# Kernel tuning notes

Measured on AMD Instinct MI355X. Metric: run time of the kernel, lower is better.

The kernel has to match this reference:

```python
import jax, jax.numpy as jnp
import numpy as np

N_NODE, N_REL = 200000, 64
DIM, N_FACTOR, N_LAYER, K, B = 64, 4, 2, 32, 1024


def setup_inputs() -> dict:
    key = jax.random.key(0)
    ks = jax.random.split(key, 12)
    node_emb = jax.random.normal(ks[0], (N_NODE, N_FACTOR, DIM), jnp.float32) * 0.05
    relation_emb = jax.random.normal(ks[1], (N_REL, N_FACTOR, DIM), jnp.float32) * 0.05
    # attention MLP: Linear(2d -> d), ReLU, Linear(d -> 1); stored as [in, out]
    W1 = jax.random.normal(ks[2], (2 * DIM, DIM), jnp.float32) * (1.0 / np.sqrt(2 * DIM))
    b1 = jnp.zeros((DIM,), jnp.float32)
    W2 = jax.random.normal(ks[3], (DIM, 1), jnp.float32) * (1.0 / np.sqrt(DIM))
    b2 = jnp.zeros((1,), jnp.float32)
    users = jax.random.randint(ks[4], (B,), 0, N_NODE)
    items = jax.random.randint(ks[5], (B,), 0, N_NODE)

    def make_triple(kh, kr, kt):
        h = jax.random.randint(kh, (B, 1, N_LAYER, K), 0, N_NODE)
        r = jax.random.randint(kr, (B, 1, N_LAYER, K), 0, N_REL)
        t = jax.random.randint(kt, (B, 1, N_LAYER, K), 0, N_NODE)
        return jnp.concatenate([h, r, t], axis=1)  # [B, 3, L, K]

    users_triple = make_triple(ks[6], ks[7], ks[8])
    items_triple = make_triple(ks[9], ks[10], ks[11])
    return {
        "node_emb": node_emb, "relation_emb": relation_emb,
        "W1": W1, "b1": b1, "W2": W2, "b2": b2,
        "users": users, "items": items,
        "users_triple": users_triple, "items_triple": items_triple,
    }


def _knowledge_attention(h_emb, t_emb, W1, b1, W2, b2):
    # h_emb, t_emb: [B, L, K, F, d]
    x = jnp.concatenate([h_emb, t_emb], axis=-1)          # [B,L,K,F,2d]
    hid = jax.nn.relu(x @ W1 + b1)                        # [B,L,K,F,d]
    logits = jnp.squeeze(hid @ W2 + b2, axis=-1)          # [B,L,K,F]
    w = jax.nn.softmax(logits, axis=2)                    # softmax over neighbors K
    return jnp.sum(w[..., None] * t_emb, axis=2)          # [B,L,F,d]


def _tower(node_emb, idx, triple, W1, b1, W2, b2):
    origin = node_emb[idx]                                # [B,F,d]
    h = node_emb[triple[:, 0]]                            # [B,L,K,F,d]
    t = node_emb[triple[:, 2]]                            # [B,L,K,F,d]
    layers = _knowledge_attention(h, t, W1, b1, W2, b2)   # [B,L,F,d]
    emb = jnp.concatenate([origin[:, None], layers], axis=1)  # [B,L+1,F,d]
    return jnp.transpose(emb, (1, 0, 2, 3))               # [L+1,B,F,d]


def reference(node_emb, relation_emb, W1, b1, W2, b2, users, items, users_triple, items_triple):
    # relation_emb is gathered in the original but never used by the attention math.
    u = _tower(node_emb, users, users_triple, W1, b1, W2, b2)
    v = _tower(node_emb, items, items_triple, W1, b1, W2, b2)
    return jnp.stack([u, v])  # [2, L+1, B, F, d]
```

## Files before the change

### kernel.cpp

```cpp
#include <hip/hip_runtime.h>
#include <math.h>

#define NNODE  200000
#define DIM    64
#define NF     4
#define NLAYER 2
#define KK     32
#define BB     1024

typedef __bf16 bf16x8 __attribute__((ext_vector_type(8)));
typedef float  f32x4  __attribute__((ext_vector_type(4)));

__global__ void prep_w1t(const float* __restrict__ W1, __bf16* __restrict__ w1t) {
    int j = blockIdx.x * 256 + threadIdx.x;
    int d = j >> 7, i = j & 127;
    w1t[j] = (__bf16)W1[i * 64 + d];
}

__global__ __launch_bounds__(256, 4) void kgat_direct(
    const float* __restrict__ node_emb,
    const __bf16* __restrict__ w1t,
    const float* __restrict__ b1,
    const float* __restrict__ W2,
    const int*   __restrict__ users,
    const int*   __restrict__ items,
    const int*   __restrict__ users_triple,
    const int*   __restrict__ items_triple,
    float*       __restrict__ out)
{
    __shared__ float logitS[128];
    __shared__ float outS[256];

    const int bid   = blockIdx.x;
    const int tower = bid >> 11;
    const int b     = (bid >> 1) & 1023;
    const int layer = bid & 1;
    const int tid   = threadIdx.x;
    const int w     = tid >> 6;
    const int lane  = tid & 63;
    const int m16   = lane & 15;
    const int quad  = lane >> 4;

    const int* __restrict__ triple = tower ? items_triple : users_triple;
    const int* __restrict__ idxarr = tower ? items : users;

    const int hbase = ((b * 3 + 0) * NLAYER + layer) * KK;
    const int tbase = ((b * 3 + 2) * NLAYER + layer) * KK;

    int hi[2], ti[2];
    hi[0] = triple[hbase + m16];
    hi[1] = triple[hbase + 16 + m16];
    ti[0] = triple[tbase + m16];
    ti[1] = triple[tbase + 16 + m16];

    bf16x8 Af[2][4];
#pragma unroll
    for (int mt = 0; mt < 2; ++mt) {
        const float* __restrict__ rh = node_emb + ((size_t)hi[mt] * NF + w) * DIM;
        const float* __restrict__ rt = node_emb + ((size_t)ti[mt] * NF + w) * DIM;
#pragma unroll
        for (int kt = 0; kt < 4; ++kt) {
            const float* __restrict__ src = (kt < 2 ? rh : rt) + (kt & 1) * 32 + quad * 8;
            f32x4 v0 = *(const f32x4*)src;
            f32x4 v1 = *(const f32x4*)(src + 4);
            bf16x8 a;
#pragma unroll
            for (int u = 0; u < 4; ++u) { a[u] = (__bf16)v0[u]; a[4 + u] = (__bf16)v1[u]; }
            Af[mt][kt] = a;
        }
    }

    f32x4 C[2][4];
#pragma unroll
    for (int mt = 0; mt < 2; ++mt)
#pragma unroll
        for (int nt = 0; nt < 4; ++nt) C[mt][nt] = (f32x4)(0.f);

#pragma unroll
    for (int kt = 0; kt < 4; ++kt) {
        bf16x8 Bn[4];
#pragma unroll
        for (int nt = 0; nt < 4; ++nt)
            Bn[nt] = *(const bf16x8*)(w1t + (nt * 16 + m16) * 128 + kt * 32 + quad * 8);
#pragma unroll
        for (int nt = 0; nt < 4; ++nt) {
            C[0][nt] = __builtin_amdgcn_mfma_f32_16x16x32_bf16(Af[0][kt], Bn[nt], C[0][nt], 0, 0, 0);
            C[1][nt] = __builtin_amdgcn_mfma_f32_16x16x32_bf16(Af[1][kt], Bn[nt], C[1][nt], 0, 0, 0);
        }
    }

    float b1v[4], w2v[4];
#pragma unroll
    for (int nt = 0; nt < 4; ++nt) {
        b1v[nt] = b1[nt * 16 + m16];
        w2v[nt] = W2[nt * 16 + m16];
    }
    float lsum[2][4];
#pragma unroll
    for (int mt = 0; mt < 2; ++mt)
#pragma unroll
        for (int r = 0; r < 4; ++r) {
            float s = 0.f;
#pragma unroll
            for (int nt = 0; nt < 4; ++nt)
                s += fmaxf(C[mt][nt][r] + b1v[nt], 0.f) * w2v[nt];
            lsum[mt][r] = s;
        }
#pragma unroll
    for (int off = 1; off < 16; off <<= 1)
#pragma unroll
        for (int mt = 0; mt < 2; ++mt)
#pragma unroll
            for (int r = 0; r < 4; ++r)
                lsum[mt][r] += __shfl_xor(lsum[mt][r], off, 64);

    if (m16 == 0) {
#pragma unroll
        for (int mt = 0; mt < 2; ++mt) {
            f32x4 v;
#pragma unroll
            for (int r = 0; r < 4; ++r) v[r] = lsum[mt][r];
            *(f32x4*)&logitS[w * 32 + mt * 16 + quad * 4] = v;
        }
    }
    const float lg = logitS[w * 32 + (lane & 31)];

    float mx = lg;
#pragma unroll
    for (int off = 16; off; off >>= 1) mx = fmaxf(mx, __shfl_xor(mx, off, 64));
    const float e = __expf(lg - mx);
    float s = e;
#pragma unroll
    for (int off = 16; off; off >>= 1) s += __shfl_xor(s, off, 64);
    const float wgt = e / s;

    float o0[8], o1[8];
#pragma unroll
    for (int j = 0; j < 8; ++j) { o0[j] = 0.f; o1[j] = 0.f; }
#pragma unroll
    for (int mt = 0; mt < 2; ++mt) {
        const float wv = __shfl(wgt, mt * 16 + m16, 64);
#pragma unroll
        for (int j = 0; j < 8; ++j) {
            o0[j] += wv * (float)Af[mt][2][j];
            o1[j] += wv * (float)Af[mt][3][j];
        }
    }
#pragma unroll
    for (int off = 1; off < 16; off <<= 1)
#pragma unroll
        for (int j = 0; j < 8; ++j) {
            o0[j] += __shfl_xor(o0[j], off, 64);
            o1[j] += __shfl_xor(o1[j], off, 64);
        }
    if (m16 == 0) {
        f32x4 v;
#pragma unroll
        for (int j = 0; j < 4; ++j) v[j] = o0[j];
        *(f32x4*)&outS[w * 64 + quad * 8] = v;
#pragma unroll
        for (int j = 0; j < 4; ++j) v[j] = o0[4 + j];
        *(f32x4*)&outS[w * 64 + quad * 8 + 4] = v;
#pragma unroll
        for (int j = 0; j < 4; ++j) v[j] = o1[j];
        *(f32x4*)&outS[w * 64 + 32 + quad * 8] = v;
#pragma unroll
        for (int j = 0; j < 4; ++j) v[j] = o1[4 + j];
        *(f32x4*)&outS[w * 64 + 32 + quad * 8 + 4] = v;
    }
    out[(((size_t)(tower * 3 + 1 + layer) * BB + b) * NF + w) * DIM + lane] =
        outS[w * 64 + lane];

    if (layer == 0) {
        const int oid = idxarr[b];
        out[(((size_t)(tower * 3 + 0) * BB + b) * NF + w) * DIM + lane] =
            node_emb[((size_t)oid * NF + w) * DIM + lane];
    }
}

extern "C" void kernel_launch(void* const* d_in, const int* in_sizes, int n_in,
                              void* d_out, int out_size, void* d_ws, size_t ws_size,
                              hipStream_t stream) {
    const float* node_emb     = (const float*)d_in[0];
    const float* W1           = (const float*)d_in[2];
    const float* b1           = (const float*)d_in[3];
    const float* W2           = (const float*)d_in[4];
    const float* b2           = (const float*)d_in[5]; (void)b2;
    const int*   users        = (const int*)d_in[6];
    const int*   items        = (const int*)d_in[7];
    const int*   users_triple = (const int*)d_in[8];
    const int*   items_triple = (const int*)d_in[9];
    float* out = (float*)d_out;

    __bf16* w1t = (__bf16*)d_ws;

    hipLaunchKernelGGL(prep_w1t, dim3(32), dim3(256), 0, stream, W1, w1t);
    hipLaunchKernelGGL(kgat_direct, dim3(2 * BB * NLAYER), dim3(256), 0, stream,
                       node_emb, w1t, b1, W2,
                       users, items, users_triple, items_triple, out);
}
```

Baseline: 304.0 us.

## Process both layers per block with prefetch of next layer's gathers

Each block now handles both layers for one (tower, batch) pair instead of one layer. The gather of layer 1's head and tail rows is issued before layer 0's compute, so memory latency overlaps with the MFMA and softmax work. W1 fragments are loaded once into registers and reused across both layers, and the LDS staging of outputs is replaced by direct vector stores from lane 0 of each 16-lane group. In exchange the grid is halved, register pressure rises (launch bounds drop from 4 to 3 blocks per CU), and a dead Bn load is left in.

```diff
diff --git a/kernel.cpp b/kernel.cpp
--- a/kernel.cpp
+++ b/kernel.cpp
@@ -17,7 +17,7 @@
     w1t[j] = (__bf16)W1[i * 64 + d];
 }
 
-__global__ __launch_bounds__(256, 4) void kgat_direct(
+__global__ __launch_bounds__(256, 3) void kgat_pipe(
     const float* __restrict__ node_emb,
     const __bf16* __restrict__ w1t,
     const float* __restrict__ b1,
@@ -29,12 +29,10 @@
     float*       __restrict__ out)
 {
     __shared__ float logitS[128];
-    __shared__ float outS[256];
 
     const int bid   = blockIdx.x;
-    const int tower = bid >> 11;
-    const int b     = (bid >> 1) & 1023;
-    const int layer = bid & 1;
+    const int tower = bid >> 10;
+    const int b     = bid & 1023;
     const int tid   = threadIdx.x;
     const int w     = tid >> 6;
     const int lane  = tid & 63;
@@ -44,138 +42,171 @@
     const int* __restrict__ triple = tower ? items_triple : users_triple;
     const int* __restrict__ idxarr = tower ? items : users;
 
-    const int hbase = ((b * 3 + 0) * NLAYER + layer) * KK;
-    const int tbase = ((b * 3 + 2) * NLAYER + layer) * KK;
-
-    int hi[2], ti[2];
-    hi[0] = triple[hbase + m16];
-    hi[1] = triple[hbase + 16 + m16];
-    ti[0] = triple[tbase + m16];
-    ti[1] = triple[tbase + 16 + m16];
-
-    bf16x8 Af[2][4];
-#pragma unroll
-    for (int mt = 0; mt < 2; ++mt) {
-        const float* __restrict__ rh = node_emb + ((size_t)hi[mt] * NF + w) * DIM;
-        const float* __restrict__ rt = node_emb + ((size_t)ti[mt] * NF + w) * DIM;
-#pragma unroll
-        for (int kt = 0; kt < 4; ++kt) {
-            const float* __restrict__ src = (kt < 2 ? rh : rt) + (kt & 1) * 32 + quad * 8;
-            f32x4 v0 = *(const f32x4*)src;
-            f32x4 v1 = *(const f32x4*)(src + 4);
-            bf16x8 a;
-#pragma unroll
-            for (int u = 0; u < 4; ++u) { a[u] = (__bf16)v0[u]; a[4 + u] = (__bf16)v1[u]; }
-            Af[mt][kt] = a;
-        }
-    }
-
-    f32x4 C[2][4];
-#pragma unroll
-    for (int mt = 0; mt < 2; ++mt)
-#pragma unroll
-        for (int nt = 0; nt < 4; ++nt) C[mt][nt] = (f32x4)(0.f);
-
-#pragma unroll
-    for (int kt = 0; kt < 4; ++kt) {
-        bf16x8 Bn[4];
-#pragma unroll
-        for (int nt = 0; nt < 4; ++nt)
-            Bn[nt] = *(const bf16x8*)(w1t + (nt * 16 + m16) * 128 + kt * 32 + quad * 8);
-#pragma unroll
-        for (int nt = 0; nt < 4; ++nt) {
-            C[0][nt] = __builtin_amdgcn_mfma_f32_16x16x32_bf16(Af[0][kt], Bn[nt], C[0][nt], 0, 0, 0);
-            C[1][nt] = __builtin_amdgcn_mfma_f32_16x16x32_bf16(Af[1][kt], Bn[nt], C[1][nt], 0, 0, 0);
-        }
-    }
-
+    int hi[NLAYER][2], ti[NLAYER][2];
+#pragma unroll
+    for (int u = 0; u < NLAYER; ++u) {
+        const int hb = ((b * 3 + 0) * NLAYER + u) * KK;
+        const int tb = ((b * 3 + 2) * NLAYER + u) * KK;
+        hi[u][0] = triple[hb + m16];
+        hi[u][1] = triple[hb + 16 + m16];
+        ti[u][0] = triple[tb + m16];
+        ti[u][1] = triple[tb + 16 + m16];
+    }
+    const int oid = idxarr[b];
+
+    bf16x8 Bn[4];
+#pragma unroll
+    for (int nt = 0; nt < 4; ++nt)
+        Bn[nt] = *(const bf16x8*)(w1t + (nt * 16 + m16) * 128 + quad * 8);
+    bf16x8 Bf[4][4];
+#pragma unroll
+    for (int nt = 0; nt < 4; ++nt)
+#pragma unroll
+        for (int kt = 0; kt < 4; ++kt)
+            Bf[nt][kt] = *(const bf16x8*)(w1t + (nt * 16 + m16) * 128 + kt * 32 + quad * 8);
     float b1v[4], w2v[4];
 #pragma unroll
     for (int nt = 0; nt < 4; ++nt) {
         b1v[nt] = b1[nt * 16 + m16];
         w2v[nt] = W2[nt * 16 + m16];
     }
-    float lsum[2][4];
-#pragma unroll
-    for (int mt = 0; mt < 2; ++mt)
-#pragma unroll
-        for (int r = 0; r < 4; ++r) {
-            float s = 0.f;
-#pragma unroll
-            for (int nt = 0; nt < 4; ++nt)
-                s += fmaxf(C[mt][nt][r] + b1v[nt], 0.f) * w2v[nt];
-            lsum[mt][r] = s;
-        }
-#pragma unroll
-    for (int off = 1; off < 16; off <<= 1)
+
+    const float orv = node_emb[((size_t)oid * NF + w) * DIM + lane];
+
+    f32x4 L[2][16];
+
+#pragma unroll
+    for (int mt = 0; mt < 2; ++mt) {
+        const float* __restrict__ rh = node_emb + ((size_t)hi[0][mt] * NF + w) * DIM;
+        const float* __restrict__ rt = node_emb + ((size_t)ti[0][mt] * NF + w) * DIM;
+#pragma unroll
+        for (int kt = 0; kt < 4; ++kt) {
+            const float* __restrict__ src = (kt < 2 ? rh : rt) + (kt & 1) * 32 + quad * 8;
+            L[0][mt * 8 + kt * 2 + 0] = *(const f32x4*)src;
+            L[0][mt * 8 + kt * 2 + 1] = *(const f32x4*)(src + 4);
+        }
+    }
+
+#pragma unroll
+    for (int u = 0; u < NLAYER; ++u) {
+        if (u + 1 < NLAYER) {
+#pragma unroll
+            for (int mt = 0; mt < 2; ++mt) {
+                const float* __restrict__ rh = node_emb + ((size_t)hi[u + 1][mt] * NF + w) * DIM;
+                const float* __restrict__ rt = node_emb + ((size_t)ti[u + 1][mt] * NF + w) * DIM;
+#pragma unroll
+                for (int kt = 0; kt < 4; ++kt) {
+                    const float* __restrict__ src = (kt < 2 ? rh : rt) + (kt & 1) * 32 + quad * 8;
+                    L[u + 1][mt * 8 + kt * 2 + 0] = *(const f32x4*)src;
+                    L[u + 1][mt * 8 + kt * 2 + 1] = *(const f32x4*)(src + 4);
+                }
+            }
+        }
+
+        bf16x8 Af[2][4];
 #pragma unroll
         for (int mt = 0; mt < 2; ++mt)
 #pragma unroll
-            for (int r = 0; r < 4; ++r)
-                lsum[mt][r] += __shfl_xor(lsum[mt][r], off, 64);
-
-    if (m16 == 0) {
+            for (int kt = 0; kt < 4; ++kt) {
+                f32x4 v0 = L[u][mt * 8 + kt * 2 + 0];
+                f32x4 v1 = L[u][mt * 8 + kt * 2 + 1];
+                bf16x8 a;
+#pragma unroll
+                for (int t = 0; t < 4; ++t) { a[t] = (__bf16)v0[t]; a[4 + t] = (__bf16)v1[t]; }
+                Af[mt][kt] = a;
+            }
+
+        f32x4 C[2][4];
+#pragma unroll
+        for (int mt = 0; mt < 2; ++mt)
+#pragma unroll
+            for (int nt = 0; nt < 4; ++nt) C[mt][nt] = (f32x4)(0.f);
+#pragma unroll
+        for (int kt = 0; kt < 4; ++kt)
+#pragma unroll
+            for (int nt = 0; nt < 4; ++nt) {
+                C[0][nt] = __builtin_amdgcn_mfma_f32_16x16x32_bf16(Af[0][kt], Bf[nt][kt], C[0][nt], 0, 0, 0);
+                C[1][nt] = __builtin_amdgcn_mfma_f32_16x16x32_bf16(Af[1][kt], Bf[nt][kt], C[1][nt], 0, 0, 0);
+            }
+
+        float lsum[2][4];
+#pragma unroll
+        for (int mt = 0; mt < 2; ++mt)
+#pragma unroll
+            for (int r = 0; r < 4; ++r) {
+                float s = 0.f;
+#pragma unroll
+                for (int nt = 0; nt < 4; ++nt)
+                    s += fmaxf(C[mt][nt][r] + b1v[nt], 0.f) * w2v[nt];
+                lsum[mt][r] = s;
+            }
+#pragma unroll
+        for (int off = 1; off < 16; off <<= 1)
+#pragma unroll
+            for (int mt = 0; mt < 2; ++mt)
+#pragma unroll
+                for (int r = 0; r < 4; ++r)
+                    lsum[mt][r] += __shfl_xor(lsum[mt][r], off, 64);
+
+        if (m16 == 0) {
+#pragma unroll
+            for (int mt = 0; mt < 2; ++mt) {
+                f32x4 v;
+#pragma unroll
+                for (int r = 0; r < 4; ++r) v[r] = lsum[mt][r];
+                *(f32x4*)&logitS[w * 32 + mt * 16 + quad * 4] = v;
+            }
+        }
+        const float lg = logitS[w * 32 + (lane & 31)];
+
+        float mx = lg;
+#pragma unroll
+        for (int off = 16; off; off >>= 1) mx = fmaxf(mx, __shfl_xor(mx, off, 64));
+        const float e = __expf(lg - mx);
+        float s = e;
+#pragma unroll
+        for (int off = 16; off; off >>= 1) s += __shfl_xor(s, off, 64);
+        const float wgt = e / s;
+
+        float o0[8], o1[8];
+#pragma unroll
+        for (int j = 0; j < 8; ++j) { o0[j] = 0.f; o1[j] = 0.f; }
 #pragma unroll
         for (int mt = 0; mt < 2; ++mt) {
+            const float wv = __shfl(wgt, mt * 16 + m16, 64);
+#pragma unroll
+            for (int j = 0; j < 8; ++j) {
+                o0[j] += wv * (float)Af[mt][2][j];
+                o1[j] += wv * (float)Af[mt][3][j];
+            }
+        }
+#pragma unroll
+        for (int off = 1; off < 16; off <<= 1)
+#pragma unroll
+            for (int j = 0; j < 8; ++j) {
+                o0[j] += __shfl_xor(o0[j], off, 64);
+                o1[j] += __shfl_xor(o1[j], off, 64);
+            }
+        if (m16 == 0) {
+            float* __restrict__ op =
+                out + (((size_t)(tower * 3 + 1 + u) * BB + b) * NF + w) * DIM;
             f32x4 v;
 #pragma unroll
-            for (int r = 0; r < 4; ++r) v[r] = lsum[mt][r];
-            *(f32x4*)&logitS[w * 32 + mt * 16 + quad * 4] = v;
-        }
-    }
-    const float lg = logitS[w * 32 + (lane & 31)];
-
-    float mx = lg;
-#pragma unroll
-    for (int off = 16; off; off >>= 1) mx = fmaxf(mx, __shfl_xor(mx, off, 64));
-    const float e = __expf(lg - mx);
-    float s = e;
-#pragma unroll
-    for (int off = 16; off; off >>= 1) s += __shfl_xor(s, off, 64);
-    const float wgt = e / s;
-
-    float o0[8], o1[8];
-#pragma unroll
-    for (int j = 0; j < 8; ++j) { o0[j] = 0.f; o1[j] = 0.f; }
-#pragma unroll
-    for (int mt = 0; mt < 2; ++mt) {
-        const float wv = __shfl(wgt, mt * 16 + m16, 64);
-#pragma unroll
-        for (int j = 0; j < 8; ++j) {
-            o0[j] += wv * (float)Af[mt][2][j];
-            o1[j] += wv * (float)Af[mt][3][j];
-        }
-    }
-#pragma unroll
-    for (int off = 1; off < 16; off <<= 1)
-#pragma unroll
-        for (int j = 0; j < 8; ++j) {
-            o0[j] += __shfl_xor(o0[j], off, 64);
-            o1[j] += __shfl_xor(o1[j], off, 64);
-        }
-    if (m16 == 0) {
-        f32x4 v;
-#pragma unroll
-        for (int j = 0; j < 4; ++j) v[j] = o0[j];
-        *(f32x4*)&outS[w * 64 + quad * 8] = v;
-#pragma unroll
-        for (int j = 0; j < 4; ++j) v[j] = o0[4 + j];
-        *(f32x4*)&outS[w * 64 + quad * 8 + 4] = v;
-#pragma unroll
-        for (int j = 0; j < 4; ++j) v[j] = o1[j];
-        *(f32x4*)&outS[w * 64 + 32 + quad * 8] = v;
-#pragma unroll
-        for (int j = 0; j < 4; ++j) v[j] = o1[4 + j];
-        *(f32x4*)&outS[w * 64 + 32 + quad * 8 + 4] = v;
-    }
-    out[(((size_t)(tower * 3 + 1 + layer) * BB + b) * NF + w) * DIM + lane] =
-        outS[w * 64 + lane];
-
-    if (layer == 0) {
-        const int oid = idxarr[b];
-        out[(((size_t)(tower * 3 + 0) * BB + b) * NF + w) * DIM + lane] =
-            node_emb[((size_t)oid * NF + w) * DIM + lane];
-    }
+            for (int j = 0; j < 4; ++j) v[j] = o0[j];
+            *(f32x4*)(op + quad * 8) = v;
+#pragma unroll
+            for (int j = 0; j < 4; ++j) v[j] = o0[4 + j];
+            *(f32x4*)(op + quad * 8 + 4) = v;
+#pragma unroll
+            for (int j = 0; j < 4; ++j) v[j] = o1[j];
+            *(f32x4*)(op + 32 + quad * 8) = v;
+#pragma unroll
+            for (int j = 0; j < 4; ++j) v[j] = o1[4 + j];
+            *(f32x4*)(op + 32 + quad * 8 + 4) = v;
+        }
+    }
+
+    out[(((size_t)(tower * 3 + 0) * BB + b) * NF + w) * DIM + lane] = orv;
 }
 
 extern "C" void kernel_launch(void* const* d_in, const int* in_sizes, int n_in,
@@ -195,7 +226,7 @@
     __bf16* w1t = (__bf16*)d_ws;
 
     hipLaunchKernelGGL(prep_w1t, dim3(32), dim3(256), 0, stream, W1, w1t);
-    hipLaunchKernelGGL(kgat_direct, dim3(2 * BB * NLAYER), dim3(256), 0, stream,
+    hipLaunchKernelGGL(kgat_pipe, dim3(2 * BB), dim3(256), 0, stream,
                        node_emb, w1t, b1, W2,
                        users, items, users_triple, items_triple, out);
 }
```

New measurement: 328.7 us. 8.1% more time.

## Stage gathered neighbor rows into LDS via async global_load_lds

Applied to the files above, without the earlier changes.

Gathers the 64 head/tail node rows (1 KB each) per block into a padded LDS buffer using async global-to-LDS loads. While those loads are in flight, the kernel preloads the W1 fragments, bias, W2 and the origin row into registers, then reads MFMA operands from LDS after a barrier. Output is written directly from registers, so the outS staging buffer and its extra pass go away. The cost is about 66 KB of LDS per block and a lower occupancy hint (2 blocks instead of 4), which may reduce latency hiding for this gather-bound kernel.

```diff
diff --git a/kernel.cpp b/kernel.cpp
--- a/kernel.cpp
+++ b/kernel.cpp
@@ -11,13 +11,15 @@
 typedef __bf16 bf16x8 __attribute__((ext_vector_type(8)));
 typedef float  f32x4  __attribute__((ext_vector_type(4)));
 
+#define RSTRIDE_DW 260
+
 __global__ void prep_w1t(const float* __restrict__ W1, __bf16* __restrict__ w1t) {
     int j = blockIdx.x * 256 + threadIdx.x;
     int d = j >> 7, i = j & 127;
     w1t[j] = (__bf16)W1[i * 64 + d];
 }
 
-__global__ __launch_bounds__(256, 4) void kgat_direct(
+__global__ __launch_bounds__(256, 2) void kgat_lds(
     const float* __restrict__ node_emb,
     const __bf16* __restrict__ w1t,
     const float* __restrict__ b1,
@@ -28,8 +30,8 @@
     const int*   __restrict__ items_triple,
     float*       __restrict__ out)
 {
+    __shared__ float Xs[64 * RSTRIDE_DW];
     __shared__ float logitS[128];
-    __shared__ float outS[256];
 
     const int bid   = blockIdx.x;
     const int tower = bid >> 11;
@@ -47,20 +49,44 @@
     const int hbase = ((b * 3 + 0) * NLAYER + layer) * KK;
     const int tbase = ((b * 3 + 2) * NLAYER + layer) * KK;
 
-    int hi[2], ti[2];
-    hi[0] = triple[hbase + m16];
-    hi[1] = triple[hbase + 16 + m16];
-    ti[0] = triple[tbase + m16];
-    ti[1] = triple[tbase + 16 + m16];
+    {
+#pragma unroll
+        for (int r8 = 0; r8 < 16; ++r8) {
+            const int r   = w * 16 + r8;
+            const int idx = (r < 32) ? triple[hbase + r] : triple[tbase + r - 32];
+            const float* gsrc = node_emb + (size_t)idx * (NF * DIM) + lane * 4;
+            __builtin_amdgcn_global_load_lds(
+                (const __attribute__((address_space(1))) void*)gsrc,
+                (__attribute__((address_space(3))) void*)&Xs[r * RSTRIDE_DW],
+                16, 0, 0);
+        }
+    }
+
+    bf16x8 Bf[4][4];
+#pragma unroll
+    for (int nt = 0; nt < 4; ++nt)
+#pragma unroll
+        for (int kt = 0; kt < 4; ++kt)
+            Bf[nt][kt] = *(const bf16x8*)(w1t + (nt * 16 + m16) * 128 + kt * 32 + quad * 8);
+    float b1v[4], w2v[4];
+#pragma unroll
+    for (int nt = 0; nt < 4; ++nt) {
+        b1v[nt] = b1[nt * 16 + m16];
+        w2v[nt] = W2[nt * 16 + m16];
+    }
+    const int oid = idxarr[b];
+    const float orv = node_emb[((size_t)oid * NF + w) * DIM + lane];
+
+    __syncthreads();
 
     bf16x8 Af[2][4];
 #pragma unroll
     for (int mt = 0; mt < 2; ++mt) {
-        const float* __restrict__ rh = node_emb + ((size_t)hi[mt] * NF + w) * DIM;
-        const float* __restrict__ rt = node_emb + ((size_t)ti[mt] * NF + w) * DIM;
+        const int e = mt * 16 + m16;
 #pragma unroll
         for (int kt = 0; kt < 4; ++kt) {
-            const float* __restrict__ src = (kt < 2 ? rh : rt) + (kt & 1) * 32 + quad * 8;
+            const int row = (kt < 2) ? e : (32 + e);
+            const float* src = &Xs[row * RSTRIDE_DW + w * 64 + (kt & 1) * 32 + quad * 8];
             f32x4 v0 = *(const f32x4*)src;
             f32x4 v1 = *(const f32x4*)(src + 4);
             bf16x8 a;
@@ -75,26 +101,14 @@
     for (int mt = 0; mt < 2; ++mt)
 #pragma unroll
         for (int nt = 0; nt < 4; ++nt) C[mt][nt] = (f32x4)(0.f);
-
-#pragma unroll
-    for (int kt = 0; kt < 4; ++kt) {
-        bf16x8 Bn[4];
-#pragma unroll
-        for (int nt = 0; nt < 4; ++nt)
-            Bn[nt] = *(const bf16x8*)(w1t + (nt * 16 + m16) * 128 + kt * 32 + quad * 8);
+#pragma unroll
+    for (int kt = 0; kt < 4; ++kt)
 #pragma unroll
         for (int nt = 0; nt < 4; ++nt) {
-            C[0][nt] = __builtin_amdgcn_mfma_f32_16x16x32_bf16(Af[0][kt], Bn[nt], C[0][nt], 0, 0, 0);
-            C[1][nt] = __builtin_amdgcn_mfma_f32_16x16x32_bf16(Af[1][kt], Bn[nt], C[1][nt], 0, 0, 0);
-        }
-    }
-
-    float b1v[4], w2v[4];
-#pragma unroll
-    for (int nt = 0; nt < 4; ++nt) {
-        b1v[nt] = b1[nt * 16 + m16];
-        w2v[nt] = W2[nt * 16 + m16];
-    }
+            C[0][nt] = __builtin_amdgcn_mfma_f32_16x16x32_bf16(Af[0][kt], Bf[nt][kt], C[0][nt], 0, 0, 0);
+            C[1][nt] = __builtin_amdgcn_mfma_f32_16x16x32_bf16(Af[1][kt], Bf[nt][kt], C[1][nt], 0, 0, 0);
+        }
+
     float lsum[2][4];
 #pragma unroll
     for (int mt = 0; mt < 2; ++mt)
@@ -154,28 +168,25 @@
             o1[j] += __shfl_xor(o1[j], off, 64);
         }
     if (m16 == 0) {
+        float* __restrict__ op =
+            out + (((size_t)(tower * 3 + 1 + layer) * BB + b) * NF + w) * DIM;
         f32x4 v;
 #pragma unroll
         for (int j = 0; j < 4; ++j) v[j] = o0[j];
-        *(f32x4*)&outS[w * 64 + quad * 8] = v;
+        *(f32x4*)(op + quad * 8) = v;
 #pragma unroll
         for (int j = 0; j < 4; ++j) v[j] = o0[4 + j];
-        *(f32x4*)&outS[w * 64 + quad * 8 + 4] = v;
+        *(f32x4*)(op + quad * 8 + 4) = v;
 #pragma unroll
         for (int j = 0; j < 4; ++j) v[j] = o1[j];
-        *(f32x4*)&outS[w * 64 + 32 + quad * 8] = v;
+        *(f32x4*)(op + 32 + quad * 8) = v;
 #pragma unroll
         for (int j = 0; j < 4; ++j) v[j] = o1[4 + j];
-        *(f32x4*)&outS[w * 64 + 32 + quad * 8 + 4] = v;
-    }
-    out[(((size_t)(tower * 3 + 1 + layer) * BB + b) * NF + w) * DIM + lane] =
-        outS[w * 64 + lane];
-
-    if (layer == 0) {
-        const int oid = idxarr[b];
-        out[(((size_t)(tower * 3 + 0) * BB + b) * NF + w) * DIM + lane] =
-            node_emb[((size_t)oid * NF + w) * DIM + lane];
-    }
+        *(f32x4*)(op + 32 + quad * 8 + 4) = v;
+    }
+
+    if (layer == 0)
+        out[(((size_t)(tower * 3 + 0) * BB + b) * NF + w) * DIM + lane] = orv;
 }
 
 extern "C" void kernel_launch(void* const* d_in, const int* in_sizes, int n_in,
@@ -195,7 +206,7 @@
     __bf16* w1t = (__bf16*)d_ws;
 
     hipLaunchKernelGGL(prep_w1t, dim3(32), dim3(256), 0, stream, W1, w1t);
-    hipLaunchKernelGGL(kgat_direct, dim3(2 * BB * NLAYER), dim3(256), 0, stream,
+    hipLaunchKernelGGL(kgat_lds, dim3(2 * BB * NLAYER), dim3(256), 0, stream,
                        node_emb, w1t, b1, W2,
                        users, items, users_triple, items_triple, out);
 }
```

After: 313.7 us. 3.2% more time.
